# Performance work log

Hardware: AMD Instinct MI355X
Metric: run time of the kernel (lower is better)

Reference implementation:

```python
import jax, jax.numpy as jnp
import numpy as np

D = 2048
N_HEAD = 16
D_HEAD = D // N_HEAD
EXP = 4
EPS = 1e-6


def setup_inputs() -> dict:
    key = jax.random.key(0)
    ks = jax.random.split(key, 8)
    b, s = 2, 2048
    scale = 0.02
    return {
        "x": jax.random.normal(ks[0], (b, s, D), dtype=jnp.float32),
        "w_qkv": jax.random.normal(ks[1], (D, 3 * D), dtype=jnp.float32) * scale,
        "w_o": jax.random.normal(ks[2], (D, D), dtype=jnp.float32) * scale,
        "w_up": jax.random.normal(ks[3], (D, EXP * D), dtype=jnp.float32) * scale,
        "w_gate": jax.random.normal(ks[4], (D, EXP * D), dtype=jnp.float32) * scale,
        "w_down": jax.random.normal(ks[5], (EXP * D, D), dtype=jnp.float32) * scale,
        "scale1": jnp.ones((D,), dtype=jnp.float32),
        "scale2": jnp.ones((D,), dtype=jnp.float32),
    }


def _rmsnorm(x, scale):
    rms = jnp.sqrt(jnp.mean(x * x, axis=-1, keepdims=True) + EPS)
    return x / rms * scale


def _attention(x, w_qkv, w_o):
    b, s, d = x.shape
    qkv = x @ w_qkv  # [b, s, 3d]
    q, k, v = jnp.split(qkv, 3, axis=-1)
    # [b, h, s, dh]
    q = q.reshape(b, s, N_HEAD, D_HEAD).transpose(0, 2, 1, 3)
    k = k.reshape(b, s, N_HEAD, D_HEAD).transpose(0, 2, 1, 3)
    v = v.reshape(b, s, N_HEAD, D_HEAD).transpose(0, 2, 1, 3)
    scores = jnp.einsum("bhqd,bhkd->bhqk", q, k) / np.sqrt(D_HEAD).astype(np.float32)
    causal = jnp.tril(jnp.ones((s, s), dtype=bool))
    scores = jnp.where(causal, scores, -jnp.inf)
    attn = jax.nn.softmax(scores, axis=-1)
    out = jnp.einsum("bhqk,bhkd->bhqd", attn, v)
    out = out.transpose(0, 2, 1, 3).reshape(b, s, d)
    return out @ w_o


def _mlp(x, w_up, w_gate, w_down):
    return (x @ w_up * jax.nn.silu(x @ w_gate)) @ w_down


def reference(x, w_qkv, w_o, w_up, w_gate, w_down, scale1, scale2):
    x = x + _attention(_rmsnorm(x, scale1), w_qkv, w_o)
    x = x + _mlp(_rmsnorm(x, scale2), w_up, w_gate, w_down)
    return x
```

## Files before the change

### kernel.cpp

```cpp
#include <hip/hip_runtime.h>

typedef unsigned short u16;
typedef __bf16 bfrag8 __attribute__((ext_vector_type(8)));
typedef float f32x4 __attribute__((ext_vector_type(4)));

#define MFMA16(a, b, c) __builtin_amdgcn_mfma_f32_16x16x32_bf16((a), (b), (c), 0, 0, 0)

static __device__ __forceinline__ u16 bf_bits(float f) {
  unsigned int u = __builtin_bit_cast(unsigned int, f);
  unsigned int r = (u + 0x7fffu + ((u >> 16) & 1u)) >> 16;
  return (u16)r;
}
static __device__ __forceinline__ float f_from_bits(u16 u) {
  unsigned int w = ((unsigned int)u) << 16;
  return __builtin_bit_cast(float, w);
}
static __device__ __forceinline__ void gload16(const void* g, void* l) {
  __builtin_amdgcn_global_load_lds(
      (const __attribute__((address_space(1))) void*)g,
      (__attribute__((address_space(3))) void*)l, 16, 0, 0);
}

__global__ __launch_bounds__(256) void k_transpose_bf16(const float* __restrict__ src,
                                                        u16* __restrict__ dst,
                                                        int K, int N) {
  __shared__ float tile[32][33];
  const int n0 = blockIdx.x * 32;
  const int k0 = blockIdx.y * 32;
  const int t = threadIdx.x;
  const int lr = t >> 5;
  const int lc = t & 31;
#pragma unroll
  for (int i = 0; i < 4; ++i)
    tile[lr + i * 8][lc] = src[(size_t)(k0 + lr + i * 8) * N + n0 + lc];
  __syncthreads();
#pragma unroll
  for (int i = 0; i < 4; ++i)
    dst[(size_t)(n0 + lr + i * 8) * K + k0 + lc] = bf_bits(tile[lc][lr + i * 8]);
}

__global__ __launch_bounds__(256) void k_transpose_v(const u16* __restrict__ qkv,
                                                     u16* __restrict__ vtg) {
  __shared__ u16 tile[32][33];
  const int bh = blockIdx.z, b = bh >> 4, hh = bh & 15;
  const int s0 = blockIdx.x * 32, d0 = blockIdx.y * 32;
  const int t = threadIdx.x;
  const int lr = t >> 5, lc = t & 31;
#pragma unroll
  for (int i = 0; i < 4; ++i)
    tile[lr + i * 8][lc] =
        qkv[(size_t)(b * 2048 + s0 + lr + i * 8) * 6144 + 4096 + hh * 128 + d0 + lc];
  __syncthreads();
#pragma unroll
  for (int i = 0; i < 4; ++i)
    vtg[(size_t)bh * 128 * 2048 + (size_t)(d0 + lr + i * 8) * 2048 + s0 + lc] =
        tile[lc][lr + i * 8];
}

__global__ __launch_bounds__(256) void k_rmsnorm(const float* __restrict__ x,
                                                 const float* __restrict__ sc,
                                                 u16* __restrict__ o) {
  const int row = blockIdx.x;
  const int t = threadIdx.x;
  const float4* x4 = (const float4*)(x + (size_t)row * 2048);
  float4 a = x4[t];
  float4 b = x4[t + 256];
  float ss = a.x * a.x + a.y * a.y + a.z * a.z + a.w * a.w +
             b.x * b.x + b.y * b.y + b.z * b.z + b.w * b.w;
#pragma unroll
  for (int off = 32; off > 0; off >>= 1) ss += __shfl_down(ss, off);
  __shared__ float red[4];
  if ((t & 63) == 0) red[t >> 6] = ss;
  __syncthreads();
  const float inv = rsqrtf((red[0] + red[1] + red[2] + red[3]) * (1.0f / 2048.0f) + 1e-6f);
  const float4* s4 = (const float4*)sc;
  float4 sa = s4[t], sb = s4[t + 256];
  ushort4 pa, pb;
  pa.x = bf_bits(a.x * inv * sa.x); pa.y = bf_bits(a.y * inv * sa.y);
  pa.z = bf_bits(a.z * inv * sa.z); pa.w = bf_bits(a.w * inv * sa.w);
  pb.x = bf_bits(b.x * inv * sb.x); pb.y = bf_bits(b.y * inv * sb.y);
  pb.z = bf_bits(b.z * inv * sb.z); pb.w = bf_bits(b.w * inv * sb.w);
  *(ushort4*)(o + (size_t)row * 2048 + t * 4) = pa;
  *(ushort4*)(o + (size_t)row * 2048 + (t + 256) * 4) = pb;
}

#define LDA(SB, H, MF, KH)                                                       \
  (*(const bfrag8*)(smC + (SB) * 65536 + (H) * 16384 +                           \
                    (wm * 64 + (MF) * 16 + l15) * 128 + (((KH) * 64 + lhi16) ^ swz)))
#define LDB(SB, NF, KH)                                                          \
  (*(const bfrag8*)(smC + (SB) * 65536 + 32768 +                                 \
                    (wn * 64 + (NF) * 16 + l15) * 128 + (((KH) * 64 + lhi16) ^ swz)))
#define STAGE_A(SB, H, KT)                                                       \
  {                                                                              \
    const u16* s_ = Asrc + (size_t)(H) * AhK + (size_t)(KT) * 64;                \
    char* d_ = smC + (SB) * 65536 + (H) * 16384 + wchunk;                        \
    gload16(s_, d_);                                                             \
    gload16(s_ + K8, d_ + 1024);                                                 \
  }
#define STAGE_B(SB, C, KT)                                                       \
  {                                                                              \
    const u16* s_ = Bsrc + (size_t)(C) * BcK + (size_t)(KT) * 64;                \
    char* d_ = smC + (SB) * 65536 + 32768 + (C) * 16384 + wchunk;                \
    gload16(s_, d_);                                                             \
    gload16(s_ + K8, d_ + 1024);                                                 \
  }
#define MM(H, I, J, AF, BF) acc[(H) * 4 + (I)][J] = MFMA16(AF, BF, acc[(H) * 4 + (I)][J])
#define PHASE(SB, H, KH, STAGE_STMT, TAIL_VM)                                    \
  {                                                                              \
    bfrag8 a0_ = LDA(SB, H, 0, KH), a1_ = LDA(SB, H, 1, KH),                     \
           a2_ = LDA(SB, H, 2, KH), a3_ = LDA(SB, H, 3, KH);                     \
    bfrag8 b0_ = LDB(SB, 0, KH), b1_ = LDB(SB, 1, KH),                           \
           b2_ = LDB(SB, 2, KH), b3_ = LDB(SB, 3, KH);                           \
    STAGE_STMT;                                                                  \
    __builtin_amdgcn_s_barrier();                                                \
    asm volatile("s_waitcnt lgkmcnt(0)" ::: "memory");                           \
    __builtin_amdgcn_sched_barrier(0);                                           \
    __builtin_amdgcn_s_setprio(1);                                               \
    MM(H, 0, 0, a0_, b0_); MM(H, 0, 1, a0_, b1_);                                \
    MM(H, 0, 2, a0_, b2_); MM(H, 0, 3, a0_, b3_);                                \
    MM(H, 1, 0, a1_, b0_); MM(H, 1, 1, a1_, b1_);                                \
    MM(H, 1, 2, a1_, b2_); MM(H, 1, 3, a1_, b3_);                                \
    MM(H, 2, 0, a2_, b0_); MM(H, 2, 1, a2_, b1_);                                \
    MM(H, 2, 2, a2_, b2_); MM(H, 2, 3, a2_, b3_);                                \
    MM(H, 3, 0, a3_, b0_); MM(H, 3, 1, a3_, b1_);                                \
    MM(H, 3, 2, a3_, b2_); MM(H, 3, 3, a3_, b3_);                                \
    __builtin_amdgcn_s_setprio(0);                                               \
    TAIL_VM;                                                                     \
    __builtin_amdgcn_s_barrier();                                                \
    asm volatile("" ::: "memory");                                               \
    __builtin_amdgcn_sched_barrier(0);                                           \
  }
#define VM2                                                                      \
  {                                                                              \
    asm volatile("s_waitcnt vmcnt(2)" ::: "memory");                             \
    __builtin_amdgcn_sched_barrier(0);                                           \
  }
#define NOPVM (void)0

template <int EPI>
__global__ __launch_bounds__(512, 1) void k_gemm8(const u16* __restrict__ A,
                                                  const u16* __restrict__ Bt,
                                                  int M, int N, int K,
                                                  float* __restrict__ outF,
                                                  u16* __restrict__ outB,
                                                  const float* __restrict__ resid,
                                                  const u16* __restrict__ gate) {
  __shared__ u16 sm[2 * 32768];
  char* smC = (char*)sm;
  const int t = threadIdx.x;
  const int m0 = blockIdx.y * 256;
  const int n0 = blockIdx.x * 256;
  const int wid = t >> 6, lane = t & 63;
  const int wm = wid >> 2, wn = wid & 3;
  const int l15 = lane & 15, lhi = lane >> 4;
  const int lhi16 = lhi * 16;
  const int swz = (l15 & 7) << 4;

  f32x4 acc[8][4];
#pragma unroll
  for (int i = 0; i < 8; ++i)
#pragma unroll
    for (int j = 0; j < 4; ++j) acc[i][j] = (f32x4){0.f, 0.f, 0.f, 0.f};

  const int sr = lane >> 3;
  const int csw = ((lane & 7) * 16 ^ (sr << 4)) >> 1;
  const u16* Asrc = A + (size_t)(m0 + (wid >> 2) * 128 + (wid & 3) * 16 + sr) * K + csw;
  const u16* Bsrc = Bt + (size_t)(n0 + wid * 16 + sr) * K + csw;
  const unsigned wchunk = (unsigned)wid * 2048 + (unsigned)lane * 16;
  const size_t K8 = (size_t)8 * K;
  const size_t AhK = (size_t)64 * K;
  const size_t BcK = (size_t)128 * K;

  const int NT = K >> 6;

  STAGE_A(0, 0, 0);
  STAGE_B(0, 0, 0);
  STAGE_B(0, 1, 0);
  STAGE_A(0, 1, 0);
  STAGE_A(1, 0, 1);
  VM2;
  __builtin_amdgcn_s_barrier();
  asm volatile("" ::: "memory");
  __builtin_amdgcn_sched_barrier(0);

  for (int it = 0; it < (NT >> 1); ++it) {
    const int kt1 = 2 * it + 1;
    const int kt2 = (2 * it + 2 < NT) ? 2 * it + 2 : NT - 1;
    const int kt3 = (2 * it + 3 < NT) ? 2 * it + 3 : NT - 1;
    PHASE(0, 0, 0, STAGE_A(1, 1, kt1), NOPVM);
    PHASE(0, 1, 0, STAGE_B(1, 0, kt1), NOPVM);
    PHASE(0, 0, 1, STAGE_B(1, 1, kt1), NOPVM);
    PHASE(0, 1, 1, STAGE_A(0, 0, kt2), VM2);
    PHASE(1, 0, 0, STAGE_B(0, 0, kt2), NOPVM);
    PHASE(1, 1, 0, STAGE_B(0, 1, kt2), NOPVM);
    PHASE(1, 0, 1, STAGE_A(0, 1, kt2), NOPVM);
    PHASE(1, 1, 1, STAGE_A(1, 0, kt3), VM2);
  }

#pragma unroll
  for (int mf = 0; mf < 8; ++mf) {
#pragma unroll
    for (int nf = 0; nf < 4; ++nf) {
      const int mr = m0 + wm * 128 + mf * 16 + lhi * 4;
      const int nc = n0 + wn * 64 + nf * 16 + l15;
#pragma unroll
      for (int r = 0; r < 4; ++r) {
        const size_t idx = (size_t)(mr + r) * N + nc;
        const float v = acc[mf][nf][r];
        if (EPI == 0) {
          outB[idx] = bf_bits(v);
        } else if (EPI == 1) {
          outF[idx] = resid[idx] + v;
        } else {
          float g = f_from_bits(gate[idx]);
          float s = g / (1.f + __expf(-g));
          outB[idx] = bf_bits(v * s);
        }
      }
    }
  }
}

__global__ __launch_bounds__(512) void k_attn(const u16* __restrict__ qkv,
                                              const u16* __restrict__ vtg,
                                              u16* __restrict__ out) {
  const int S = 2048, LD = 6144;
  const float scale = 0.0883883476483184405f;
  const int bh = blockIdx.y;
  const int b = bh >> 4, hh = bh & 15;
  const int qt = (b == 0) ? (15 - (int)blockIdx.x) : (int)blockIdx.x;
  const int t = threadIdx.x;
  const int wave = t >> 6, lane = t & 63;
  const int l15 = lane & 15, lhi = lane >> 4;
  const int lhi16 = lhi * 16;
  const int swz = (l15 & 7) << 4;

  __shared__ u16 Kt[64 * 128];
  __shared__ u16 Vt[128 * 64];
  __shared__ u16 Pl[8][16][72];
  char* KtC = (char*)Kt;
  char* VtC = (char*)Vt;

  const int qrow = qt * 128 + wave * 16 + l15;
  const size_t qoff = (size_t)(b * S + qrow) * LD + hh * 128 + lhi * 8;
  bfrag8 qf[4];
#pragma unroll
  for (int ks = 0; ks < 4; ++ks) qf[ks] = *(const bfrag8*)(qkv + qoff + ks * 32);

  f32x4 oacc[8];
#pragma unroll
  for (int j = 0; j < 8; ++j) oacc[j] = (f32x4){0.f, 0.f, 0.f, 0.f};
  float m_i[4], l_i[4];
#pragma unroll
  for (int r = 0; r < 4; ++r) { m_i[r] = -INFINITY; l_i[r] = 0.f; }

  const int q_my = qt * 128 + wave * 16 + lhi * 4;
  const int q_wave_last = qt * 128 + wave * 16 + 15;

  const int keyA = t >> 4, keyB = 32 + (t >> 4);
  const int oK = (t & 15) * 16;
  const int dA = t >> 3, dB = 64 + (t >> 3);
  const int oV = (t & 7) * 16;
  const u16* kbase = qkv + (size_t)(b * S) * LD + 2048 + hh * 128;
  const u16* vbase = vtg + (size_t)bh * 128 * S;
  const u16* ksrcA = kbase + (size_t)keyA * LD + ((oK ^ ((keyA & 7) << 4)) >> 1);
  const u16* ksrcB = kbase + (size_t)keyB * LD + ((oK ^ ((keyB & 7) << 4)) >> 1);
  const u16* vsrcA = vbase + (size_t)dA * S + ((oV ^ ((dA & 7) << 4)) >> 1);
  const u16* vsrcB = vbase + (size_t)dB * S + ((oV ^ ((dB & 7) << 4)) >> 1);
  const unsigned int ldso0 = wave * 1024 + lane * 16;
  const unsigned int ldso1 = 8192 + wave * 1024 + lane * 16;
  const size_t kstep = (size_t)64 * LD;

  const int kt_max = 2 * qt + 1;
  for (int kt = 0; kt <= kt_max; ++kt) {
    __syncthreads();
    gload16(ksrcA + (size_t)kt * kstep, KtC + ldso0);
    gload16(ksrcB + (size_t)kt * kstep, KtC + ldso1);
    gload16(vsrcA + kt * 64, VtC + ldso0);
    gload16(vsrcB + kt * 64, VtC + ldso1);
    __syncthreads();

    if (kt * 64 <= q_wave_last) {
      f32x4 sfr[4];
#pragma unroll
      for (int j = 0; j < 4; ++j) {
        sfr[j] = (f32x4){0.f, 0.f, 0.f, 0.f};
        const int krow = j * 16 + l15;
#pragma unroll
        for (int ks = 0; ks < 4; ++ks) {
          bfrag8 kf = *(const bfrag8*)(KtC + krow * 256 + ((ks * 64 + lhi16) ^ swz));
          sfr[j] = MFMA16(qf[ks], kf, sfr[j]);
        }
      }
      float sv[4][4], rmax[4];
#pragma unroll
      for (int r = 0; r < 4; ++r) rmax[r] = -INFINITY;
#pragma unroll
      for (int j = 0; j < 4; ++j) {
        const int key = kt * 64 + j * 16 + l15;
#pragma unroll
        for (int r = 0; r < 4; ++r) {
          float v = sfr[j][r] * scale;
          v = (key <= q_my + r) ? v : -INFINITY;
          sv[j][r] = v;
          rmax[r] = fmaxf(rmax[r], v);
        }
      }
#pragma unroll
      for (int r = 0; r < 4; ++r) {
        float v = rmax[r];
        v = fmaxf(v, __shfl_xor(v, 1));
        v = fmaxf(v, __shfl_xor(v, 2));
        v = fmaxf(v, __shfl_xor(v, 4));
        v = fmaxf(v, __shfl_xor(v, 8));
        rmax[r] = v;
      }
      float alpha[4], rsum[4];
#pragma unroll
      for (int r = 0; r < 4; ++r) {
        float mn = fmaxf(m_i[r], rmax[r]);
        alpha[r] = __expf(m_i[r] - mn);
        m_i[r] = mn;
        rsum[r] = 0.f;
      }
#pragma unroll
      for (int j = 0; j < 4; ++j) {
#pragma unroll
        for (int r = 0; r < 4; ++r) {
          float p = __expf(sv[j][r] - m_i[r]);
          rsum[r] += p;
          Pl[wave][lhi * 4 + r][j * 16 + l15] = bf_bits(p);
        }
      }
#pragma unroll
      for (int r = 0; r < 4; ++r) {
        float v = rsum[r];
        v += __shfl_xor(v, 1); v += __shfl_xor(v, 2);
        v += __shfl_xor(v, 4); v += __shfl_xor(v, 8);
        l_i[r] = l_i[r] * alpha[r] + v;
      }
#pragma unroll
      for (int j = 0; j < 8; ++j)
#pragma unroll
        for (int r = 0; r < 4; ++r) oacc[j][r] *= alpha[r];

#pragma unroll
      for (int ks2 = 0; ks2 < 2; ++ks2) {
        bfrag8 pf = *(const bfrag8*)&Pl[wave][l15][ks2 * 32 + lhi * 8];
#pragma unroll
        for (int j = 0; j < 8; ++j) {
          const int d = j * 16 + l15;
          bfrag8 vf = *(const bfrag8*)(VtC + d * 128 + ((ks2 * 64 + lhi16) ^ swz));
          oacc[j] = MFMA16(pf, vf, oacc[j]);
        }
      }
    }
  }

#pragma unroll
  for (int r = 0; r < 4; ++r) {
    const float inv = 1.f / l_i[r];
    const size_t tok = (size_t)b * S + qt * 128 + wave * 16 + lhi * 4 + r;
#pragma unroll
    for (int j = 0; j < 8; ++j)
      out[tok * 2048 + hh * 128 + j * 16 + l15] = bf_bits(oacc[j][r] * inv);
  }
}

extern "C" void kernel_launch(void* const* d_in, const int* in_sizes, int n_in,
                              void* d_out, int out_size, void* d_ws, size_t ws_size,
                              hipStream_t stream) {
  (void)in_sizes; (void)n_in; (void)out_size; (void)ws_size;
  const float* x      = (const float*)d_in[0];
  const float* w_qkv  = (const float*)d_in[1];
  const float* w_o    = (const float*)d_in[2];
  const float* w_up   = (const float*)d_in[3];
  const float* w_gate = (const float*)d_in[4];
  const float* w_down = (const float*)d_in[5];
  const float* scale1 = (const float*)d_in[6];
  const float* scale2 = (const float*)d_in[7];
  float* out = (float*)d_out;

  u16* B       = (u16*)d_ws;
  u16* wqkvT   = B;
  u16* woT     = wqkvT  + (size_t)6144 * 2048;
  u16* wgateT  = woT    + (size_t)2048 * 2048;
  u16* wupT    = wgateT + (size_t)8192 * 2048;
  u16* wdownT  = wupT   + (size_t)8192 * 2048;
  u16* xn      = wdownT + (size_t)2048 * 8192;
  u16* qkvb    = xn     + (size_t)4096 * 2048;
  u16* attnb   = qkvb   + (size_t)4096 * 6144;
  float* y1    = (float*)(attnb + (size_t)4096 * 2048);
  u16* vtg     = (u16*)y1;
  u16* gbuf    = qkvb;
  u16* hbuf    = wqkvT;

  dim3 blk(256);
  k_transpose_bf16<<<dim3(192, 64), blk, 0, stream>>>(w_qkv,  wqkvT,  2048, 6144);
  k_transpose_bf16<<<dim3(64, 64),  blk, 0, stream>>>(w_o,    woT,    2048, 2048);
  k_transpose_bf16<<<dim3(256, 64), blk, 0, stream>>>(w_gate, wgateT, 2048, 8192);
  k_transpose_bf16<<<dim3(256, 64), blk, 0, stream>>>(w_up,   wupT,   2048, 8192);
  k_transpose_bf16<<<dim3(64, 256), blk, 0, stream>>>(w_down, wdownT, 8192, 2048);

  k_rmsnorm<<<4096, blk, 0, stream>>>(x, scale1, xn);
  k_gemm8<0><<<dim3(24, 16), dim3(512), 0, stream>>>(xn, wqkvT, 4096, 6144, 2048, nullptr, qkvb, nullptr, nullptr);
  k_transpose_v<<<dim3(64, 4, 32), blk, 0, stream>>>(qkvb, vtg);
  k_attn<<<dim3(16, 32), dim3(512), 0, stream>>>(qkvb, vtg, attnb);
  k_gemm8<1><<<dim3(8, 16), dim3(512), 0, stream>>>(attnb, woT, 4096, 2048, 2048, y1, nullptr, x, nullptr);
  k_rmsnorm<<<4096, blk, 0, stream>>>(y1, scale2, xn);
  k_gemm8<0><<<dim3(32, 16), dim3(512), 0, stream>>>(xn, wgateT, 4096, 8192, 2048, nullptr, gbuf, nullptr, nullptr);
  k_gemm8<2><<<dim3(32, 16), dim3(512), 0, stream>>>(xn, wupT, 4096, 8192, 2048, nullptr, hbuf, nullptr, gbuf);
  k_gemm8<1><<<dim3(8, 16), dim3(512), 0, stream>>>(hbuf, wdownT, 4096, 2048, 8192, out, nullptr, y1, nullptr);
}
```

Baseline: 908.6 us.

## Template GEMM on K, remap blocks across XCDs, relax waits and raise occupancy bound

The GEMM kernel takes K as a template parameter so address strides become compile-time constants. Workgroup ids are remapped so consecutive tiles group by XCD, which should improve L2 reuse. The explicit lgkmcnt wait and several sched_barriers are removed so the compiler schedules LDS reads against the MFMAs itself, and launch_bounds changes from (512,1) to (512,2). The relaxed waits rely on compiler-inserted waitcnts, and the higher occupancy bound may squeeze the 128-register accumulator and force spills.

After: 915.4 us. No clear change (+0.7%).

```diff
diff --git a/kernel.cpp b/kernel.cpp
--- a/kernel.cpp
+++ b/kernel.cpp
@@ -92,17 +92,17 @@
                     (wn * 64 + (NF) * 16 + l15) * 128 + (((KH) * 64 + lhi16) ^ swz)))
 #define STAGE_A(SB, H, KT)                                                       \
   {                                                                              \
-    const u16* s_ = Asrc + (size_t)(H) * AhK + (size_t)(KT) * 64;                \
+    const u16* s_ = Asrc + (size_t)(H) * (64 * K) + (size_t)(KT) * 64;           \
     char* d_ = smC + (SB) * 65536 + (H) * 16384 + wchunk;                        \
     gload16(s_, d_);                                                             \
-    gload16(s_ + K8, d_ + 1024);                                                 \
+    gload16(s_ + 8 * K, d_ + 1024);                                              \
   }
 #define STAGE_B(SB, C, KT)                                                       \
   {                                                                              \
-    const u16* s_ = Bsrc + (size_t)(C) * BcK + (size_t)(KT) * 64;                \
+    const u16* s_ = Bsrc + (size_t)(C) * (128 * K) + (size_t)(KT) * 64;          \
     char* d_ = smC + (SB) * 65536 + 32768 + (C) * 16384 + wchunk;                \
     gload16(s_, d_);                                                             \
-    gload16(s_ + K8, d_ + 1024);                                                 \
+    gload16(s_ + 8 * K, d_ + 1024);                                              \
   }
 #define MM(H, I, J, AF, BF) acc[(H) * 4 + (I)][J] = MFMA16(AF, BF, acc[(H) * 4 + (I)][J])
 #define PHASE(SB, H, KH, STAGE_STMT, TAIL_VM)                                    \
@@ -113,8 +113,6 @@
            b2_ = LDB(SB, 2, KH), b3_ = LDB(SB, 3, KH);                           \
     STAGE_STMT;                                                                  \
     __builtin_amdgcn_s_barrier();                                                \
-    asm volatile("s_waitcnt lgkmcnt(0)" ::: "memory");                           \
-    __builtin_amdgcn_sched_barrier(0);                                           \
     __builtin_amdgcn_s_setprio(1);                                               \
     MM(H, 0, 0, a0_, b0_); MM(H, 0, 1, a0_, b1_);                                \
     MM(H, 0, 2, a0_, b2_); MM(H, 0, 3, a0_, b3_);                                \
@@ -127,20 +125,14 @@
     __builtin_amdgcn_s_setprio(0);                                               \
     TAIL_VM;                                                                     \
     __builtin_amdgcn_s_barrier();                                                \
-    asm volatile("" ::: "memory");                                               \
-    __builtin_amdgcn_sched_barrier(0);                                           \
-  }
-#define VM2                                                                      \
-  {                                                                              \
-    asm volatile("s_waitcnt vmcnt(2)" ::: "memory");                             \
-    __builtin_amdgcn_sched_barrier(0);                                           \
-  }
+  }
+#define VM2 asm volatile("s_waitcnt vmcnt(2)" ::: "memory")
 #define NOPVM (void)0
 
-template <int EPI>
-__global__ __launch_bounds__(512, 1) void k_gemm8(const u16* __restrict__ A,
+template <int EPI, int K>
+__global__ __launch_bounds__(512, 2) void k_gemm8(const u16* __restrict__ A,
                                                   const u16* __restrict__ Bt,
-                                                  int M, int N, int K,
+                                                  int M, int N,
                                                   float* __restrict__ outF,
                                                   u16* __restrict__ outB,
                                                   const float* __restrict__ resid,
@@ -148,8 +140,13 @@
   __shared__ u16 sm[2 * 32768];
   char* smC = (char*)sm;
   const int t = threadIdx.x;
-  const int m0 = blockIdx.y * 256;
-  const int n0 = blockIdx.x * 256;
+  const int nbx = gridDim.x;
+  const int nwg = nbx * gridDim.y;
+  int f = blockIdx.x + nbx * blockIdx.y;
+  f = (f & 7) * (nwg >> 3) + (f >> 3);
+  const int m0 = (f / nbx) * 256;
+  const int n0 = (f % nbx) * 256;
+
   const int wid = t >> 6, lane = t & 63;
   const int wm = wid >> 2, wn = wid & 3;
   const int l15 = lane & 15, lhi = lane >> 4;
@@ -163,25 +160,21 @@
     for (int j = 0; j < 4; ++j) acc[i][j] = (f32x4){0.f, 0.f, 0.f, 0.f};
 
   const int sr = lane >> 3;
-  const int csw = ((lane & 7) * 16 ^ (sr << 4)) >> 1;
-  const u16* Asrc = A + (size_t)(m0 + (wid >> 2) * 128 + (wid & 3) * 16 + sr) * K + csw;
+  const int csw = (((lane & 7) * 16) ^ (sr << 4)) >> 1;
+  const u16* Asrc =
+      A + (size_t)(m0 + (wid >> 2) * 128 + (wid & 3) * 16 + sr) * K + csw;
   const u16* Bsrc = Bt + (size_t)(n0 + wid * 16 + sr) * K + csw;
   const unsigned wchunk = (unsigned)wid * 2048 + (unsigned)lane * 16;
-  const size_t K8 = (size_t)8 * K;
-  const size_t AhK = (size_t)64 * K;
-  const size_t BcK = (size_t)128 * K;
 
   const int NT = K >> 6;
 
   STAGE_A(0, 0, 0);
+  STAGE_A(0, 1, 0);
   STAGE_B(0, 0, 0);
   STAGE_B(0, 1, 0);
-  STAGE_A(0, 1, 0);
   STAGE_A(1, 0, 1);
   VM2;
   __builtin_amdgcn_s_barrier();
-  asm volatile("" ::: "memory");
-  __builtin_amdgcn_sched_barrier(0);
 
   for (int it = 0; it < (NT >> 1); ++it) {
     const int kt1 = 2 * it + 1;
@@ -403,12 +396,12 @@
   k_transpose_bf16<<<dim3(64, 256), blk, 0, stream>>>(w_down, wdownT, 8192, 2048);
 
   k_rmsnorm<<<4096, blk, 0, stream>>>(x, scale1, xn);
-  k_gemm8<0><<<dim3(24, 16), dim3(512), 0, stream>>>(xn, wqkvT, 4096, 6144, 2048, nullptr, qkvb, nullptr, nullptr);
+  k_gemm8<0, 2048><<<dim3(24, 16), dim3(512), 0, stream>>>(xn, wqkvT, 4096, 6144, nullptr, qkvb, nullptr, nullptr);
   k_transpose_v<<<dim3(64, 4, 32), blk, 0, stream>>>(qkvb, vtg);
   k_attn<<<dim3(16, 32), dim3(512), 0, stream>>>(qkvb, vtg, attnb);
-  k_gemm8<1><<<dim3(8, 16), dim3(512), 0, stream>>>(attnb, woT, 4096, 2048, 2048, y1, nullptr, x, nullptr);
+  k_gemm8<1, 2048><<<dim3(8, 16), dim3(512), 0, stream>>>(attnb, woT, 4096, 2048, y1, nullptr, x, nullptr);
   k_rmsnorm<<<4096, blk, 0, stream>>>(y1, scale2, xn);
-  k_gemm8<0><<<dim3(32, 16), dim3(512), 0, stream>>>(xn, wgateT, 4096, 8192, 2048, nullptr, gbuf, nullptr, nullptr);
-  k_gemm8<2><<<dim3(32, 16), dim3(512), 0, stream>>>(xn, wupT, 4096, 8192, 2048, nullptr, hbuf, nullptr, gbuf);
-  k_gemm8<1><<<dim3(8, 16), dim3(512), 0, stream>>>(hbuf, wdownT, 4096, 2048, 8192, out, nullptr, y1, nullptr);
-}
+  k_gemm8<0, 2048><<<dim3(32, 16), dim3(512), 0, stream>>>(xn, wgateT, 4096, 8192, nullptr, gbuf, nullptr, nullptr);
+  k_gemm8<2, 2048><<<dim3(32, 16), dim3(512), 0, stream>>>(xn, wupT, 4096, 8192, nullptr, hbuf, nullptr, gbuf);
+  k_gemm8<1, 8192><<<dim3(8, 16), dim3(512), 0, stream>>>(hbuf, wdownT, 4096, 2048, out, nullptr, y1, nullptr);
+}
```
